# Kernel tuning notes

Measured on AMD Instinct MI355X. Metric: run time of the kernel, lower is better.

## Reference

```python
import jax, jax.numpy as jnp
import numpy as np

B, N, H = 8, 1024, 768
NH, HD = 12, 64  # num heads, head size
E = 131072       # total edges (avg degree 16)
N_REL = 30


def setup_inputs() -> dict:
    key = jax.random.key(0)
    ks = jax.random.split(key, 8)
    node_states = jax.random.normal(ks[0], (B, N, H), dtype=jnp.float32)
    eb = jax.random.randint(ks[1], (E,), 0, B, dtype=jnp.int32)
    ei = jax.random.randint(ks[2], (E,), 0, N, dtype=jnp.int32)
    ej = jax.random.randint(ks[3], (E,), 0, N, dtype=jnp.int32)
    er = jax.random.randint(ks[4], (E,), 0, N_REL, dtype=jnp.int32)
    edge_indices = jnp.stack([eb, ei, ej, er], axis=0)  # (4, E)
    scale = 1.0 / np.sqrt(H)
    Wq = jax.random.normal(ks[5], (H, H), dtype=jnp.float32) * scale
    Wk = jax.random.normal(ks[6], (H, H), dtype=jnp.float32) * scale
    Wv = jax.random.normal(ks[7], (H, H), dtype=jnp.float32) * scale
    return {"node_states": node_states, "edge_indices": edge_indices,
            "Wq": Wq, "Wk": Wk, "Wv": Wv}


def reference(node_states, edge_indices, Wq, Wk, Wv):
    # node_states: (B, N, H); edge_indices: (4, E) rows = (batch, head_node, tail_node, relation)
    b, i, j = edge_indices[0], edge_indices[1], edge_indices[2]
    q = (node_states @ Wq).reshape(B, N, NH, HD)
    k = (node_states @ Wk).reshape(B, N, NH, HD)
    v = (node_states @ Wv).reshape(B, N, NH, HD)
    qe = q[b, i]  # (E, NH, HD) gather at head nodes
    ke = k[b, j]  # (E, NH, HD) gather at tail nodes
    scores = jnp.einsum('ehd,ehd->eh', qe, ke) * (1.0 / np.sqrt(HD))  # (E, NH)
    seg = b * N + i  # segment = (batch, head_node)
    nseg = B * N
    smax = jax.ops.segment_max(scores, seg, num_segments=nseg)  # (nseg, NH)
    ex = jnp.exp(scores - smax[seg])
    denom = jax.ops.segment_sum(ex, seg, num_segments=nseg)
    probs = ex / jnp.maximum(denom[seg], 1e-9)  # (E, NH) edge softmax over tail nodes
    ve = v[b, j]  # (E, NH, HD)
    out_e = (probs[:, :, None] * ve).reshape(E, NH * HD)
    out = jax.ops.segment_sum(out_e, seg, num_segments=nseg)  # sum over tail dim
    return out.reshape(B, N, H)
```

## Files before the change

kernel.cpp:

```cpp
#include <hip/hip_runtime.h>
#include <hip/hip_fp16.h>

#define BB 8
#define NN 1024
#define HH 768
#define NHEAD 12
#define HD 64
#define NSEG 8192
#define QKVN 2304
#define MAXDEG 64

typedef unsigned short u16;
typedef __attribute__((ext_vector_type(8))) _Float16 f16x8;
typedef __attribute__((ext_vector_type(4))) float f32x4;
typedef __attribute__((ext_vector_type(4))) unsigned int u32x4;
typedef __attribute__((ext_vector_type(2))) unsigned int u32x2;

__device__ __forceinline__ u16 f2h(float f) {
  _Float16 h = (_Float16)f;
  return __builtin_bit_cast(u16, h);
}
__device__ __forceinline__ __half2 h2(unsigned int w) {
  return __builtin_bit_cast(__half2, w);
}

#define CAST_BLKS (NSEG * HH / 4 / 256)
#define TW_BLKS   ((QKVN / 32) * (HH / 32))
#define BUILD_BLKS 512

__global__ void prep_kernel(const float* __restrict__ X, u16* __restrict__ Xb,
                            const float* __restrict__ Wq, const float* __restrict__ Wk,
                            const float* __restrict__ Wv, u16* __restrict__ Wt,
                            const int* __restrict__ EI, int* __restrict__ cursor,
                            int* __restrict__ tailrow, int E) {
  const int bid = blockIdx.x;
  if (bid < CAST_BLKS) {
    int i = bid * 256 + threadIdx.x;
    float4 f = ((const float4*)X)[i];
    ushort4 o;
    o.x = f2h(f.x); o.y = f2h(f.y); o.z = f2h(f.z); o.w = f2h(f.w);
    ((ushort4*)Xb)[i] = o;
  } else if (bid < CAST_BLKS + TW_BLKS) {
    __shared__ float tile[32][33];
    int t = bid - CAST_BLKS;
    int n0 = (t % (QKVN / 32)) * 32;
    int k0 = (t / (QKVN / 32)) * 32;
    const float* W = (n0 < HH) ? Wq : (n0 < 2 * HH ? Wk : Wv);
    int nb = n0 - (n0 < HH ? 0 : (n0 < 2 * HH ? HH : 2 * HH));
    int tx = threadIdx.x & 31, ty = threadIdx.x >> 5;
#pragma unroll
    for (int r = 0; r < 4; ++r)
      tile[ty + 8 * r][tx] = W[(k0 + ty + 8 * r) * HH + nb + tx];
    __syncthreads();
#pragma unroll
    for (int r = 0; r < 4; ++r)
      Wt[(n0 + ty + 8 * r) * HH + k0 + tx] = f2h(tile[tx][ty + 8 * r]);
  } else {
    int e = (bid - CAST_BLKS - TW_BLKS) * 256 + threadIdx.x;
    if (e >= E) return;
    int b = EI[e];
    int seg = b * NN + EI[E + e];
    int j = EI[2 * E + e];
    int pos = atomicAdd(&cursor[seg], 1);
    if (pos < MAXDEG) tailrow[seg * MAXDEG + pos] = b * NN + j;
  }
}

#define GBM 256
#define GBN 128
#define GBK 64
#define GNT (HH / GBK)

__global__ __launch_bounds__(512, 2) void gemm_kernel(const u16* __restrict__ Xb,
                                                      const u16* __restrict__ Wt,
                                                      u16* __restrict__ QKV) {
  __shared__ u16 As[3][GBM * GBK];
  __shared__ u16 Bs[3][GBN * GBK];
  const int tid = threadIdx.x;
  const int wave = tid >> 6;
  const int lane = tid & 63;
  const int quad = lane >> 4;
  const int l15 = lane & 15;
  const int wr = wave >> 1;
  const int wc = wave & 1;

  const int bid = blockIdx.x;
  const int wgid = (bid & 7) * 72 + (bid >> 3);
  const int mt = wgid / 18;
  const int nt = wgid % 18;
  const int m0 = mt * GBM;
  const int n0 = nt * GBN;

  f32x4 acc[4][4] = {};

  auto stage_half = [&](int buf, int kt, int h) {
#pragma unroll
    for (int iss = 0; iss < 2; ++iss) {
      const int c = (wave * 4 + h * 2 + iss) * 64 + lane;
      const int m = c >> 3;
      const u16* ga = Xb + (m0 + m) * HH + kt + (((c & 7) ^ (m & 7)) << 3);
      u16* la = &As[buf][c * 8];
      __builtin_amdgcn_global_load_lds(
          (const __attribute__((address_space(1))) unsigned int*)(unsigned long long)ga,
          (__attribute__((address_space(3))) unsigned int*)(unsigned long long)la, 16, 0, 0);
    }
    {
      const int c = (wave * 2 + h) * 64 + lane;
      const int n = c >> 3;
      const u16* gb = Wt + (n0 + n) * HH + kt + (((c & 7) ^ (n & 7)) << 3);
      u16* lb = &Bs[buf][c * 8];
      __builtin_amdgcn_global_load_lds(
          (const __attribute__((address_space(1))) unsigned int*)(unsigned long long)gb,
          (__attribute__((address_space(3))) unsigned int*)(unsigned long long)lb, 16, 0, 0);
    }
  };

  stage_half(0, 0, 0);
  stage_half(0, 0, 1);
  stage_half(1, GBK, 0);
  stage_half(1, GBK, 1);

#pragma unroll 3
  for (int it = 0; it < GNT; ++it) {
    if (it != GNT - 1) {
      asm volatile("s_waitcnt vmcnt(6)" ::: "memory");
    } else {
      asm volatile("s_waitcnt vmcnt(0)" ::: "memory");
    }
    __builtin_amdgcn_s_barrier();
    const int b = it % 3;
    const int nb2 = (it + 2) % 3;
    const bool pre = (it + 2) < GNT;
    const int ktn = (it + 2) * GBK;

#pragma unroll
    for (int ks = 0; ks < 2; ++ks) {
      f16x8 afr[4], bfr[4];
#pragma unroll
      for (int mi = 0; mi < 4; ++mi) {
        const int m = wr * 64 + mi * 16 + l15;
        afr[mi] = *(const f16x8*)(&As[b][m * GBK + ((((ks << 2) | quad) ^ (m & 7)) << 3)]);
      }
#pragma unroll
      for (int ni = 0; ni < 4; ++ni) {
        const int n = wc * 64 + ni * 16 + l15;
        bfr[ni] = *(const f16x8*)(&Bs[b][n * GBK + ((((ks << 2) | quad) ^ (n & 7)) << 3)]);
      }
      if (pre) stage_half(nb2, ktn, ks);
      __builtin_amdgcn_s_barrier();
      asm volatile("s_waitcnt lgkmcnt(0)" ::: "memory");
      __builtin_amdgcn_sched_barrier(0);
      __builtin_amdgcn_s_setprio(1);
#pragma unroll
      for (int mi = 0; mi < 4; ++mi)
#pragma unroll
        for (int ni = 0; ni < 4; ++ni)
          acc[mi][ni] = __builtin_amdgcn_mfma_f32_16x16x32_f16(afr[mi], bfr[ni], acc[mi][ni], 0, 0, 0);
      __builtin_amdgcn_s_setprio(0);
      if (ks == 0) __builtin_amdgcn_s_barrier();
    }
  }

#pragma unroll
  for (int mi = 0; mi < 4; ++mi)
#pragma unroll
    for (int ni = 0; ni < 4; ++ni) {
      const int col = n0 + wc * 64 + ni * 16 + l15;
#pragma unroll
      for (int r = 0; r < 4; ++r) {
        const int row = m0 + wr * 64 + mi * 16 + quad * 4 + r;
        QKV[row * QKVN + col] = f2h(acc[mi][ni][r]);
      }
    }
}

__global__ __launch_bounds__(256) void attn_kernel(const u16* __restrict__ QKV,
                                                   const int* __restrict__ tailrow,
                                                   const int* __restrict__ cursor,
                                                   float* __restrict__ out) {
  __shared__ float sm[3 * 16 * 64];
  const int wv = threadIdx.x >> 6;
  const int lane = threadIdx.x & 63;
  const int seg = (blockIdx.x & 7) * (NSEG / 8) + (blockIdx.x >> 3);
  const int base = seg * MAXDEG;
  int cnt = cursor[seg];
  if (cnt > MAXDEG) cnt = MAXDEG;
  const int myn = (cnt > wv) ? ((cnt - wv + 3) >> 2) : 0;

  int myidx = (lane < cnt) ? tailrow[base + lane] : 0;

  const u16* qrow = QKV + seg * QKVN;
  __half2 q1[4], q2[2];
  {
    u32x4 qa = *(const u32x4*)(qrow + lane * 8);
    u32x2 qb = *(const u32x2*)(qrow + 512 + lane * 4);
    const __half2 sc = __float2half2_rn(0.125f);
#pragma unroll
    for (int i = 0; i < 4; ++i) q1[i] = __hmul2(h2(qa[i]), sc);
    q2[0] = __hmul2(h2(qb[0]), sc);
    q2[1] = __hmul2(h2(qb[1]), sc);
  }

  float m1 = -__builtin_inff(), l1 = 0.f;
  float m2 = -__builtin_inff(), l2 = 0.f;
  __half2 o1[4] = {}, o2[2] = {};

  auto loadkv = [&](int row, u32x4& k1, u32x2& k2, u32x4& v1, u32x2& v2) {
    const u16* kp = QKV + row * QKVN + HH;
    k1 = *(const u32x4*)(kp + lane * 8);
    k2 = *(const u32x2*)(kp + 512 + lane * 4);
    v1 = *(const u32x4*)(kp + HH + lane * 8);
    v2 = *(const u32x2*)(kp + HH + 512 + lane * 4);
  };

  auto process = [&](u32x4 k1, u32x2 k2, u32x4 v1, u32x2 v2) {
    __half2 a1 = __hmul2(q1[0], h2(k1[0]));
    a1 = __hfma2(q1[1], h2(k1[1]), a1);
    a1 = __hfma2(q1[2], h2(k1[2]), a1);
    a1 = __hfma2(q1[3], h2(k1[3]), a1);
    float s1 = __low2float(a1) + __high2float(a1);
    s1 += __shfl_xor(s1, 1, 64);
    s1 += __shfl_xor(s1, 2, 64);
    s1 += __shfl_xor(s1, 4, 64);
    __half2 a2 = __hmul2(q2[0], h2(k2[0]));
    a2 = __hfma2(q2[1], h2(k2[1]), a2);
    float s2 = __low2float(a2) + __high2float(a2);
    s2 += __shfl_xor(s2, 1, 64);
    s2 += __shfl_xor(s2, 2, 64);
    s2 += __shfl_xor(s2, 4, 64);
    s2 += __shfl_xor(s2, 8, 64);
    {
      float mn = fmaxf(m1, s1);
      float al = __expf(m1 - mn);
      float ex = __expf(s1 - mn);
      l1 = l1 * al + ex;
      __half2 ah = __float2half2_rn(al), eh = __float2half2_rn(ex);
#pragma unroll
      for (int i = 0; i < 4; ++i)
        o1[i] = __hfma2(o1[i], ah, __hmul2(h2(v1[i]), eh));
      m1 = mn;
    }
    {
      float mn = fmaxf(m2, s2);
      float al = __expf(m2 - mn);
      float ex = __expf(s2 - mn);
      l2 = l2 * al + ex;
      __half2 ah = __float2half2_rn(al), eh = __float2half2_rn(ex);
      o2[0] = __hfma2(o2[0], ah, __hmul2(h2(v2[0]), eh));
      o2[1] = __hfma2(o2[1], ah, __hmul2(h2(v2[1]), eh));
      m2 = mn;
    }
  };

  if (myn > 0) {
    u32x4 k1c, v1c, k1n, v1n, k1n2, v1n2;
    u32x2 k2c, v2c, k2n, v2n, k2n2, v2n2;
    loadkv(__shfl(myidx, wv, 64), k1c, k2c, v1c, v2c);
    if (myn > 1) loadkv(__shfl(myidx, wv + 4, 64), k1n, k2n, v1n, v2n);
    for (int t = 0; t < myn; ++t) {
      if (t + 2 < myn)
        loadkv(__shfl(myidx, wv + 4 * (t + 2), 64), k1n2, k2n2, v1n2, v2n2);
      process(k1c, k2c, v1c, v2c);
      k1c = k1n; k2c = k2n; v1c = v1n; v2c = v2n;
      k1n = k1n2; k2n = k2n2; v1n = v1n2; v2n = v2n2;
    }
  }

  float of1[8], of2[4];
#pragma unroll
  for (int i = 0; i < 4; ++i) {
    of1[2 * i] = __low2float(o1[i]);
    of1[2 * i + 1] = __high2float(o1[i]);
  }
#pragma unroll
  for (int i = 0; i < 2; ++i) {
    of2[2 * i] = __low2float(o2[i]);
    of2[2 * i + 1] = __high2float(o2[i]);
  }

  if (wv > 0) {
    float* sb = sm + (wv - 1) * 1024;
    sb[0 * 64 + lane] = m1;  sb[1 * 64 + lane] = l1;
    sb[2 * 64 + lane] = m2;  sb[3 * 64 + lane] = l2;
#pragma unroll
    for (int i = 0; i < 8; ++i) sb[(4 + i) * 64 + lane] = of1[i];
#pragma unroll
    for (int i = 0; i < 4; ++i) sb[(12 + i) * 64 + lane] = of2[i];
  }
  __syncthreads();
  if (wv == 0) {
    float mn1 = fmaxf(m1, -1e30f), mn2 = fmaxf(m2, -1e30f);
#pragma unroll
    for (int j = 0; j < 3; ++j) {
      mn1 = fmaxf(mn1, sm[j * 1024 + 0 * 64 + lane]);
      mn2 = fmaxf(mn2, sm[j * 1024 + 2 * 64 + lane]);
    }
    float res1[8], res2[4];
    {
      float a0 = __expf(m1 - mn1);
      float l = l1 * a0;
#pragma unroll
      for (int i = 0; i < 8; ++i) res1[i] = of1[i] * a0;
#pragma unroll
      for (int j = 0; j < 3; ++j) {
        const float* sb = sm + j * 1024;
        float aj = __expf(sb[0 * 64 + lane] - mn1);
        l += sb[1 * 64 + lane] * aj;
#pragma unroll
        for (int i = 0; i < 8; ++i) res1[i] += sb[(4 + i) * 64 + lane] * aj;
      }
      float inv = 1.f / fmaxf(l, 1e-9f);
#pragma unroll
      for (int i = 0; i < 8; ++i) res1[i] *= inv;
    }
    {
      float a0 = __expf(m2 - mn2);
      float l = l2 * a0;
#pragma unroll
      for (int i = 0; i < 4; ++i) res2[i] = of2[i] * a0;
#pragma unroll
      for (int j = 0; j < 3; ++j) {
        const float* sb = sm + j * 1024;
        float aj = __expf(sb[2 * 64 + lane] - mn2);
        l += sb[3 * 64 + lane] * aj;
#pragma unroll
        for (int i = 0; i < 4; ++i) res2[i] += sb[(12 + i) * 64 + lane] * aj;
      }
      float inv = 1.f / fmaxf(l, 1e-9f);
#pragma unroll
      for (int i = 0; i < 4; ++i) res2[i] *= inv;
    }

    float* op = out + seg * HH;
    float4 r0 = {res1[0], res1[1], res1[2], res1[3]};
    float4 r1 = {res1[4], res1[5], res1[6], res1[7]};
    float4 r2 = {res2[0], res2[1], res2[2], res2[3]};
    ((float4*)(op + lane * 8))[0] = r0;
    ((float4*)(op + lane * 8))[1] = r1;
    *(float4*)(op + 512 + lane * 4) = r2;
  }
}

extern "C" void kernel_launch(void* const* d_in, const int* in_sizes, int n_in,
                              void* d_out, int out_size, void* d_ws, size_t ws_size,
                              hipStream_t stream) {
  const float* X  = (const float*)d_in[0];
  const int*   EI = (const int*)d_in[1];
  const float* Wq = (const float*)d_in[2];
  const float* Wk = (const float*)d_in[3];
  const float* Wv = (const float*)d_in[4];
  float* out = (float*)d_out;
  const int E = in_sizes[1] / 4;

  char* ws = (char*)d_ws;
  int* cursor  = (int*)(ws);
  int* tailrow = (int*)(ws + 32768);
  u16* Xb      = (u16*)(ws + 2129920);
  u16* Wt      = (u16*)(ws + 14712832);
  u16* QKV     = (u16*)(ws + 18251776);

  hipMemsetAsync(cursor, 0, NSEG * 4, stream);
  prep_kernel<<<CAST_BLKS + TW_BLKS + BUILD_BLKS, 256, 0, stream>>>(
      X, Xb, Wq, Wk, Wv, Wt, EI, cursor, tailrow, E);
  gemm_kernel<<<(NSEG / GBM) * (QKVN / GBN), 512, 0, stream>>>(Xb, Wt, QKV);
  attn_kernel<<<NSEG, 256, 0, stream>>>(QKV, tailrow, cursor, out);
}
```

Baseline: 177.4 us.

## Restructure QKV GEMM to four waves with 128x64 warp tiles and BK=32

The QKV projection GEMM now runs with 256 threads instead of 512. Each wave computes a 128x64 output tile with an 8x4 accumulator array, and the K step drops from 64 to 32 with a 4-way XOR swizzle adjusted to match. The goal is more register-level reuse of the B fragments per LDS load and a smaller shared-memory footprint. The costs are twice as many K iterations and barriers, and fewer resident waves to hide latency.

```diff
diff --git a/kernel.cpp b/kernel.cpp
--- a/kernel.cpp
+++ b/kernel.cpp
@@ -68,10 +68,10 @@
 
 #define GBM 256
 #define GBN 128
-#define GBK 64
+#define GBK 32
 #define GNT (HH / GBK)
 
-__global__ __launch_bounds__(512, 2) void gemm_kernel(const u16* __restrict__ Xb,
+__global__ __launch_bounds__(256, 2) void gemm_kernel(const u16* __restrict__ Xb,
                                                       const u16* __restrict__ Wt,
                                                       u16* __restrict__ QKV) {
   __shared__ u16 As[3][GBM * GBK];
@@ -81,8 +81,8 @@
   const int lane = tid & 63;
   const int quad = lane >> 4;
   const int l15 = lane & 15;
-  const int wr = wave >> 1;
-  const int wc = wave & 1;
+  const int wm = (wave >> 1) * 128;
+  const int wn = (wave & 1) * 64;
 
   const int bid = blockIdx.x;
   const int wgid = (bid & 7) * 72 + (bid >> 3);
@@ -91,23 +91,23 @@
   const int m0 = mt * GBM;
   const int n0 = nt * GBN;
 
-  f32x4 acc[4][4] = {};
-
-  auto stage_half = [&](int buf, int kt, int h) {
+  f32x4 acc[8][4] = {};
+
+  auto stage_part = [&](int buf, int kt, int p) {
 #pragma unroll
     for (int iss = 0; iss < 2; ++iss) {
-      const int c = (wave * 4 + h * 2 + iss) * 64 + lane;
-      const int m = c >> 3;
-      const u16* ga = Xb + (m0 + m) * HH + kt + (((c & 7) ^ (m & 7)) << 3);
+      const int c = (p * 2 + iss) * 256 + tid;
+      const int r = c >> 2;
+      const u16* ga = Xb + (m0 + r) * HH + kt + (((c & 3) ^ (r & 3)) << 3);
       u16* la = &As[buf][c * 8];
       __builtin_amdgcn_global_load_lds(
           (const __attribute__((address_space(1))) unsigned int*)(unsigned long long)ga,
           (__attribute__((address_space(3))) unsigned int*)(unsigned long long)la, 16, 0, 0);
     }
     {
-      const int c = (wave * 2 + h) * 64 + lane;
-      const int n = c >> 3;
-      const u16* gb = Wt + (n0 + n) * HH + kt + (((c & 7) ^ (n & 7)) << 3);
+      const int c = p * 256 + tid;
+      const int r = c >> 2;
+      const u16* gb = Wt + (n0 + r) * HH + kt + (((c & 3) ^ (r & 3)) << 3);
       u16* lb = &Bs[buf][c * 8];
       __builtin_amdgcn_global_load_lds(
           (const __attribute__((address_space(1))) unsigned int*)(unsigned long long)gb,
@@ -115,10 +115,10 @@
     }
   };
 
-  stage_half(0, 0, 0);
-  stage_half(0, 0, 1);
-  stage_half(1, GBK, 0);
-  stage_half(1, GBK, 1);
+  stage_part(0, 0, 0);
+  stage_part(0, 0, 1);
+  stage_part(1, GBK, 0);
+  stage_part(1, GBK, 1);
 
 #pragma unroll 3
   for (int it = 0; it < GNT; ++it) {
@@ -133,20 +133,23 @@
     const bool pre = (it + 2) < GNT;
     const int ktn = (it + 2) * GBK;
 
-#pragma unroll
-    for (int ks = 0; ks < 2; ++ks) {
-      f16x8 afr[4], bfr[4];
+    f16x8 bfr[4];
+#pragma unroll
+    for (int s = 0; s < 2; ++s) {
+      f16x8 afr[4];
 #pragma unroll
       for (int mi = 0; mi < 4; ++mi) {
-        const int m = wr * 64 + mi * 16 + l15;
-        afr[mi] = *(const f16x8*)(&As[b][m * GBK + ((((ks << 2) | quad) ^ (m & 7)) << 3)]);
-      }
-#pragma unroll
-      for (int ni = 0; ni < 4; ++ni) {
-        const int n = wc * 64 + ni * 16 + l15;
-        bfr[ni] = *(const f16x8*)(&Bs[b][n * GBK + ((((ks << 2) | quad) ^ (n & 7)) << 3)]);
-      }
-      if (pre) stage_half(nb2, ktn, ks);
+        const int m = wm + (s * 4 + mi) * 16 + l15;
+        afr[mi] = *(const f16x8*)(&As[b][m * GBK + ((quad ^ (m & 3)) << 3)]);
+      }
+      if (s == 0) {
+#pragma unroll
+        for (int ni = 0; ni < 4; ++ni) {
+          const int n = wn + ni * 16 + l15;
+          bfr[ni] = *(const f16x8*)(&Bs[b][n * GBK + ((quad ^ (n & 3)) << 3)]);
+        }
+      }
+      if (pre) stage_part(nb2, ktn, s);
       __builtin_amdgcn_s_barrier();
       asm volatile("s_waitcnt lgkmcnt(0)" ::: "memory");
       __builtin_amdgcn_sched_barrier(0);
@@ -155,20 +158,19 @@
       for (int mi = 0; mi < 4; ++mi)
 #pragma unroll
         for (int ni = 0; ni < 4; ++ni)
-          acc[mi][ni] = __builtin_amdgcn_mfma_f32_16x16x32_f16(afr[mi], bfr[ni], acc[mi][ni], 0, 0, 0);
+          acc[s * 4 + mi][ni] = __builtin_amdgcn_mfma_f32_16x16x32_f16(afr[mi], bfr[ni], acc[s * 4 + mi][ni], 0, 0, 0);
       __builtin_amdgcn_s_setprio(0);
-      if (ks == 0) __builtin_amdgcn_s_barrier();
-    }
-  }
-
-#pragma unroll
-  for (int mi = 0; mi < 4; ++mi)
+    }
+  }
+
+#pragma unroll
+  for (int mi = 0; mi < 8; ++mi)
 #pragma unroll
     for (int ni = 0; ni < 4; ++ni) {
-      const int col = n0 + wc * 64 + ni * 16 + l15;
+      const int col = n0 + wn + ni * 16 + l15;
 #pragma unroll
       for (int r = 0; r < 4; ++r) {
-        const int row = m0 + wr * 64 + mi * 16 + quad * 4 + r;
+        const int row = m0 + wm + mi * 16 + quad * 4 + r;
         QKV[row * QKVN + col] = f2h(acc[mi][ni][r]);
       }
     }
@@ -362,6 +364,6 @@
   hipMemsetAsync(cursor, 0, NSEG * 4, stream);
   prep_kernel<<<CAST_BLKS + TW_BLKS + BUILD_BLKS, 256, 0, stream>>>(
       X, Xb, Wq, Wk, Wv, Wt, EI, cursor, tailrow, E);
-  gemm_kernel<<<(NSEG / GBM) * (QKVN / GBN), 512, 0, stream>>>(Xb, Wt, QKV);
+  gemm_kernel<<<(NSEG / GBM) * (QKVN / GBN), 256, 0, stream>>>(Xb, Wt, QKV);
   attn_kernel<<<NSEG, 256, 0, stream>>>(QKV, tailrow, cursor, out);
 }
```

Measured after the change: 165.8 us. 1.07x faster.

## Restructure QKV GEMM pipeline to 4-stage ring with K=32 slices

Applied to the files above, without the earlier changes.

The GEMM main loop now uses a ring of four 32-wide K slices, prefetched three ahead, in place of a triple-buffered pipeline of 64-wide K tiles split into halves. The LDS swizzle changes to match the narrower rows, and the loop is peeled so the vmcnt waits line up with the outstanding loads. This aims at deeper load/compute overlap with simpler per-iteration staging. It costs twice as many barrier-delimited iterations over K.

```diff
diff --git a/kernel.cpp b/kernel.cpp
--- a/kernel.cpp
+++ b/kernel.cpp
@@ -68,21 +68,21 @@
 
 #define GBM 256
 #define GBN 128
-#define GBK 64
-#define GNT (HH / GBK)
+#define HKK 32
+#define NHALF (HH / HKK)
 
 __global__ __launch_bounds__(512, 2) void gemm_kernel(const u16* __restrict__ Xb,
                                                       const u16* __restrict__ Wt,
                                                       u16* __restrict__ QKV) {
-  __shared__ u16 As[3][GBM * GBK];
-  __shared__ u16 Bs[3][GBN * GBK];
+  __shared__ u16 As[4][GBM * HKK];
+  __shared__ u16 Bs[4][GBN * HKK];
   const int tid = threadIdx.x;
   const int wave = tid >> 6;
   const int lane = tid & 63;
   const int quad = lane >> 4;
   const int l15 = lane & 15;
-  const int wr = wave >> 1;
-  const int wc = wave & 1;
+  const int wm = (wave >> 1) * 64;
+  const int wn = (wave & 1) * 64;
 
   const int bid = blockIdx.x;
   const int wgid = (bid & 7) * 72 + (bid >> 3);
@@ -93,82 +93,80 @@
 
   f32x4 acc[4][4] = {};
 
-  auto stage_half = [&](int buf, int kt, int h) {
-#pragma unroll
-    for (int iss = 0; iss < 2; ++iss) {
-      const int c = (wave * 4 + h * 2 + iss) * 64 + lane;
-      const int m = c >> 3;
-      const u16* ga = Xb + (m0 + m) * HH + kt + (((c & 7) ^ (m & 7)) << 3);
-      u16* la = &As[buf][c * 8];
+  auto stage = [&](int h) {
+    const int slot = h & 3;
+    const int k0 = h * HKK;
+#pragma unroll
+    for (int ld = 0; ld < 2; ++ld) {
+      const int c = ld * 512 + tid;
+      const int r = c >> 2;
+      const int kq = (c & 3) ^ ((r ^ (r >> 2)) & 3);
+      const u16* ga = Xb + (m0 + r) * HH + k0 + (kq << 3);
+      u16* la = &As[slot][c * 8];
       __builtin_amdgcn_global_load_lds(
           (const __attribute__((address_space(1))) unsigned int*)(unsigned long long)ga,
           (__attribute__((address_space(3))) unsigned int*)(unsigned long long)la, 16, 0, 0);
     }
     {
-      const int c = (wave * 2 + h) * 64 + lane;
-      const int n = c >> 3;
-      const u16* gb = Wt + (n0 + n) * HH + kt + (((c & 7) ^ (n & 7)) << 3);
-      u16* lb = &Bs[buf][c * 8];
+      const int c = tid;
+      const int r = c >> 2;
+      const int kq = (c & 3) ^ ((r ^ (r >> 2)) & 3);
+      const u16* gb = Wt + (n0 + r) * HH + k0 + (kq << 3);
+      u16* lb = &Bs[slot][c * 8];
       __builtin_amdgcn_global_load_lds(
           (const __attribute__((address_space(1))) unsigned int*)(unsigned long long)gb,
           (__attribute__((address_space(3))) unsigned int*)(unsigned long long)lb, 16, 0, 0);
     }
   };
 
-  stage_half(0, 0, 0);
-  stage_half(0, 0, 1);
-  stage_half(1, GBK, 0);
-  stage_half(1, GBK, 1);
-
-#pragma unroll 3
-  for (int it = 0; it < GNT; ++it) {
-    if (it != GNT - 1) {
-      asm volatile("s_waitcnt vmcnt(6)" ::: "memory");
-    } else {
-      asm volatile("s_waitcnt vmcnt(0)" ::: "memory");
-    }
+  auto body = [&](int h, bool dostage) {
     __builtin_amdgcn_s_barrier();
-    const int b = it % 3;
-    const int nb2 = (it + 2) % 3;
-    const bool pre = (it + 2) < GNT;
-    const int ktn = (it + 2) * GBK;
-
-#pragma unroll
-    for (int ks = 0; ks < 2; ++ks) {
-      f16x8 afr[4], bfr[4];
-#pragma unroll
-      for (int mi = 0; mi < 4; ++mi) {
-        const int m = wr * 64 + mi * 16 + l15;
-        afr[mi] = *(const f16x8*)(&As[b][m * GBK + ((((ks << 2) | quad) ^ (m & 7)) << 3)]);
-      }
-#pragma unroll
-      for (int ni = 0; ni < 4; ++ni) {
-        const int n = wc * 64 + ni * 16 + l15;
-        bfr[ni] = *(const f16x8*)(&Bs[b][n * GBK + ((((ks << 2) | quad) ^ (n & 7)) << 3)]);
-      }
-      if (pre) stage_half(nb2, ktn, ks);
-      __builtin_amdgcn_s_barrier();
-      asm volatile("s_waitcnt lgkmcnt(0)" ::: "memory");
-      __builtin_amdgcn_sched_barrier(0);
-      __builtin_amdgcn_s_setprio(1);
-#pragma unroll
-      for (int mi = 0; mi < 4; ++mi)
-#pragma unroll
-        for (int ni = 0; ni < 4; ++ni)
-          acc[mi][ni] = __builtin_amdgcn_mfma_f32_16x16x32_f16(afr[mi], bfr[ni], acc[mi][ni], 0, 0, 0);
-      __builtin_amdgcn_s_setprio(0);
-      if (ks == 0) __builtin_amdgcn_s_barrier();
-    }
-  }
+    const int slot = h & 3;
+    f16x8 afr[4], bfr[4];
+#pragma unroll
+    for (int mi = 0; mi < 4; ++mi) {
+      const int m = wm + mi * 16 + l15;
+      afr[mi] = *(const f16x8*)(&As[slot][m * HKK + ((quad ^ ((m ^ (m >> 2)) & 3)) << 3)]);
+    }
+#pragma unroll
+    for (int ni = 0; ni < 4; ++ni) {
+      const int n = wn + ni * 16 + l15;
+      bfr[ni] = *(const f16x8*)(&Bs[slot][n * HKK + ((quad ^ ((n ^ (n >> 2)) & 3)) << 3)]);
+    }
+    if (dostage) stage(h + 3);
+    __builtin_amdgcn_s_barrier();
+    asm volatile("s_waitcnt lgkmcnt(0)" ::: "memory");
+    __builtin_amdgcn_sched_barrier(0);
+    __builtin_amdgcn_s_setprio(1);
+#pragma unroll
+    for (int mi = 0; mi < 4; ++mi)
+#pragma unroll
+      for (int ni = 0; ni < 4; ++ni)
+        acc[mi][ni] = __builtin_amdgcn_mfma_f32_16x16x32_f16(afr[mi], bfr[ni], acc[mi][ni], 0, 0, 0);
+    __builtin_amdgcn_s_setprio(0);
+  };
+
+  stage(0);
+  stage(1);
+  stage(2);
+
+  for (int h = 0; h < NHALF - 2; ++h) {
+    asm volatile("s_waitcnt vmcnt(6)" ::: "memory");
+    body(h, h + 3 < NHALF);
+  }
+  asm volatile("s_waitcnt vmcnt(3)" ::: "memory");
+  body(NHALF - 2, false);
+  asm volatile("s_waitcnt vmcnt(0)" ::: "memory");
+  body(NHALF - 1, false);
 
 #pragma unroll
   for (int mi = 0; mi < 4; ++mi)
 #pragma unroll
     for (int ni = 0; ni < 4; ++ni) {
-      const int col = n0 + wc * 64 + ni * 16 + l15;
+      const int col = n0 + wn + ni * 16 + l15;
 #pragma unroll
       for (int r = 0; r < 4; ++r) {
-        const int row = m0 + wr * 64 + mi * 16 + quad * 4 + r;
+        const int row = m0 + wm + mi * 16 + quad * 4 + r;
         QKV[row * QKVN + col] = f2h(acc[mi][ni][r]);
       }
     }
```

Measured after the change: 172.9 us. 2.5% less time.
